# Kernel optimization log

Hardware: AMD Instinct MI355X
Metric: run time of the kernel (lower is better)

## Reference

```python
import jax, jax.numpy as jnp
import numpy as np

B, S, D, H, DFF = 4, 2048, 2048, 16, 8192
DH = D // H
THETA = 10000.0
EPS = 1e-5


def rmsnorm(x, g):
    return x * jax.lax.rsqrt(jnp.mean(x * x, axis=-1, keepdims=True) + EPS) * g


def rope(x, pos):
    # x: [B, H, S, DH]; rotate interleaved even/odd pairs
    half = DH // 2
    inv_freq = THETA ** (-(jnp.arange(half, dtype=jnp.float32) * 2.0) / DH)  # [half]
    ang = pos.astype(jnp.float32)[:, None] * inv_freq  # [S, half]
    cos, sin = jnp.cos(ang), jnp.sin(ang)
    x1, x2 = x[..., 0::2], x[..., 1::2]
    r1 = x1 * cos - x2 * sin
    r2 = x1 * sin + x2 * cos
    return jnp.stack([r1, r2], axis=-1).reshape(x.shape)


def setup_inputs() -> dict:
    key = jax.random.key(0)
    ks = jax.random.split(key, 12)
    s = 0.02
    return {
        "x": jax.random.normal(ks[0], (B, S, D), dtype=jnp.float32),
        "attention_mask": jnp.ones((S, S), dtype=bool),
        "wq": jax.random.normal(ks[1], (D, D), dtype=jnp.float32) * s,
        "wk": jax.random.normal(ks[2], (D, D), dtype=jnp.float32) * s,
        "wv": jax.random.normal(ks[3], (D, D), dtype=jnp.float32) * s,
        "wo": jax.random.normal(ks[4], (D, D), dtype=jnp.float32) * s,
        "w1": jax.random.normal(ks[5], (DFF, D), dtype=jnp.float32) * s,
        "w2": jax.random.normal(ks[6], (D, DFF), dtype=jnp.float32) * s,
        "w3": jax.random.normal(ks[7], (DFF, D), dtype=jnp.float32) * s,
        "g1": jnp.ones((D,), dtype=jnp.float32),
        "g2": jnp.ones((D,), dtype=jnp.float32),
    }


def reference(x, attention_mask, wq, wk, wv, wo, w1, w2, w3, g1, g2):
    pos = jnp.arange(x.shape[-2])
    # pre-norm attention
    h = rmsnorm(x, g1)
    q = (h @ wq.T).reshape(B, S, H, DH).transpose(0, 2, 1, 3)
    k = (h @ wk.T).reshape(B, S, H, DH).transpose(0, 2, 1, 3)
    v = (h @ wv.T).reshape(B, S, H, DH).transpose(0, 2, 1, 3)
    q = rope(q, pos)
    k = rope(k, pos)
    scores = jnp.einsum("bhqd,bhkd->bhqk", q, k) / np.float32(np.sqrt(DH))
    scores = jnp.where(attention_mask, scores, jnp.float32(-1e9))
    attn = jax.nn.softmax(scores, axis=-1)
    o = jnp.einsum("bhqk,bhkd->bhqd", attn, v)
    o = o.transpose(0, 2, 1, 3).reshape(B, S, D) @ wo.T
    x = x + o
    # pre-norm SwiGLU FFN
    h2 = rmsnorm(x, g2)
    ffn = (jax.nn.silu(h2 @ w1.T) * (h2 @ w3.T)) @ w2.T
    return x + ffn
```

## Files before the change

kernel.cpp:

```cpp
#include <hip/hip_runtime.h>
#include <cstdint>
#include <cstddef>

#define B_   4
#define S_   2048
#define D_   2048
#define H_   16
#define DH_  128
#define DFF_ 8192
#define LOG2E 1.4426950408889634f

typedef __bf16 bf16_t;
typedef __bf16 bf16x4 __attribute__((ext_vector_type(4)));
typedef __bf16 bf16x8 __attribute__((ext_vector_type(8)));
typedef float  f32x4  __attribute__((ext_vector_type(4)));

#define MFMA16 __builtin_amdgcn_mfma_f32_16x16x32_bf16

__device__ __forceinline__ void glds16(const void* g, void* l) {
  __builtin_amdgcn_global_load_lds((__attribute__((address_space(1))) void*)g,
                                   (__attribute__((address_space(3))) void*)l,
                                   16, 0, 0);
}

__global__ __launch_bounds__(256) void cvt_kernel(const float* __restrict__ in,
                                                  bf16_t* __restrict__ out, int n8) {
  int i = blockIdx.x * 256 + threadIdx.x;
  if (i >= n8) return;
  const float4* p4 = (const float4*)in;
  float4 a = p4[2 * (size_t)i];
  float4 b = p4[2 * (size_t)i + 1];
  bf16x8 o;
  o[0] = (bf16_t)a.x; o[1] = (bf16_t)a.y; o[2] = (bf16_t)a.z; o[3] = (bf16_t)a.w;
  o[4] = (bf16_t)b.x; o[5] = (bf16_t)b.y; o[6] = (bf16_t)b.z; o[7] = (bf16_t)b.w;
  ((bf16x8*)out)[i] = o;
}

__global__ __launch_bounds__(256) void rmsnorm_kernel(const float* __restrict__ x,
                                                      const float* __restrict__ g,
                                                      bf16_t* __restrict__ out) {
  const int row = blockIdx.x, tid = threadIdx.x;
  const float* xr = x + (size_t)row * D_;
  float4 a = ((const float4*)xr)[tid * 2];
  float4 b = ((const float4*)xr)[tid * 2 + 1];
  float ss = a.x*a.x + a.y*a.y + a.z*a.z + a.w*a.w
           + b.x*b.x + b.y*b.y + b.z*b.z + b.w*b.w;
#pragma unroll
  for (int m = 1; m < 64; m <<= 1) ss += __shfl_xor(ss, m);
  __shared__ float red[4];
  if ((tid & 63) == 0) red[tid >> 6] = ss;
  __syncthreads();
  float tot = red[0] + red[1] + red[2] + red[3];
  float rms = rsqrtf(tot * (1.0f / D_) + 1e-5f);
  float4 ga = ((const float4*)g)[tid * 2];
  float4 gb = ((const float4*)g)[tid * 2 + 1];
  bf16x8 o;
  o[0] = (bf16_t)(a.x * rms * ga.x); o[1] = (bf16_t)(a.y * rms * ga.y);
  o[2] = (bf16_t)(a.z * rms * ga.z); o[3] = (bf16_t)(a.w * rms * ga.w);
  o[4] = (bf16_t)(b.x * rms * gb.x); o[5] = (bf16_t)(b.y * rms * gb.y);
  o[6] = (bf16_t)(b.z * rms * gb.z); o[7] = (bf16_t)(b.w * rms * gb.w);
  ((bf16x8*)out)[(size_t)row * 256 + tid] = o;
}


#define RD_A(d, mg)                                                           \
  do {                                                                        \
    const char* p_ = ldsb + (d) * 32768 + wm * 16384 + l15 * 128 + (mg) * 8192; \
    _Pragma("unroll") for (int i_ = 0; i_ < 4; i_++) {                        \
      afr[i_][0] = *(const bf16x8*)(p_ + i_ * 2048 + acol0);                  \
      afr[i_][1] = *(const bf16x8*)(p_ + i_ * 2048 + acol1);                  \
    }                                                                         \
  } while (0)

#define RD_B(d, ng, dst)                                                      \
  do {                                                                        \
    const char* p_ = ldsb + 65536 + (d) * 32768 + (wn >> 1) * 16384 +         \
                     ((wn & 1) * 64 + l15) * 128 + (ng) * 4096;               \
    _Pragma("unroll") for (int j_ = 0; j_ < 2; j_++) {                        \
      dst[j_][0] = *(const bf16x8*)(p_ + j_ * 2048 + acol0);                  \
      dst[j_][1] = *(const bf16x8*)(p_ + j_ * 2048 + acol1);                  \
    }                                                                         \
  } while (0)

#define STAGE_A(d, kt)                                                        \
  do {                                                                        \
    char* dst_ = ldsb + (d) * 32768 + o0;                                     \
    const bf16_t* s_ = Asrc + (size_t)(kt) * 64;                              \
    glds16(s_, dst_);                                                         \
    glds16(s_ + 64 * (size_t)K, dst_ + 8192);                                 \
    glds16(s_ + 128 * (size_t)K, dst_ + 16384);                               \
    glds16(s_ + 192 * (size_t)K, dst_ + 24576);                               \
  } while (0)

#define STAGE_B(d, kt)                                                        \
  do {                                                                        \
    char* dst_ = ldsb + 65536 + (d) * 32768 + o0;                             \
    const bf16_t* s_ = Wsrc + (size_t)(kt) * 64;                              \
    glds16(s_, dst_);                                                         \
    glds16(s_ + 64 * (size_t)K, dst_ + 8192);                                 \
    glds16(s_ + 128 * (size_t)K, dst_ + 16384);                               \
    glds16(s_ + 192 * (size_t)K, dst_ + 24576);                               \
  } while (0)

#define DO_MFMA(mg, ng, bsrc)                                                 \
  do {                                                                        \
    __builtin_amdgcn_s_setprio(1);                                            \
    _Pragma("unroll") for (int i_ = 0; i_ < 4; i_++)                          \
    _Pragma("unroll") for (int j_ = 0; j_ < 2; j_++) {                        \
      acc[(mg)*4 + i_][(ng)*2 + j_] =                                         \
          MFMA16(afr[i_][0], bsrc[j_][0], acc[(mg)*4 + i_][(ng)*2 + j_], 0,0,0); \
      acc[(mg)*4 + i_][(ng)*2 + j_] =                                         \
          MFMA16(afr[i_][1], bsrc[j_][1], acc[(mg)*4 + i_][(ng)*2 + j_], 0,0,0); \
    }                                                                         \
    __builtin_amdgcn_s_setprio(0);                                            \
  } while (0)

#define PHASE_FENCE()                                                         \
  do {                                                                        \
    __builtin_amdgcn_sched_barrier(0);                                        \
    __builtin_amdgcn_s_barrier();                                             \
  } while (0)

template <int EPI>
__global__ __launch_bounds__(512, 2) void gemm256(const bf16_t* __restrict__ A,
                                                  const bf16_t* __restrict__ W,
                                                  const float* __restrict__ addf,
                                                  const bf16_t* __restrict__ addb,
                                                  bf16_t* __restrict__ outb,
                                                  bf16_t* __restrict__ outb2,
                                                  bf16_t* __restrict__ outb3,
                                                  float* __restrict__ outf,
                                                  int M, int N, int K) {
  __shared__ char ldsb[131072];
  const int tid = threadIdx.x;
  const int wid = tid >> 6, l = tid & 63, l15 = l & 15, lg = l >> 4;
  const int wm = wid >> 2, wn = wid & 3;

  const int nwg = gridDim.x;
  int wg = (int)blockIdx.x;
  wg = (wg & 7) * (nwg >> 3) + (wg >> 3);
  const int ntn = N >> 8;
  const int m0 = (wg / ntn) << 8, n0 = (wg % ntn) << 8;

  f32x4 acc[8][4];
  const f32x4 z4 = {0.f, 0.f, 0.f, 0.f};
#pragma unroll
  for (int i = 0; i < 8; i++)
#pragma unroll
    for (int j = 0; j < 4; j++) acc[i][j] = z4;

  const int o0 = tid * 16;
  const int srow = o0 >> 7;
  const int ssw = ((o0 & 127) ^ ((srow & 7) << 4)) >> 1;
  const bf16_t* Asrc = A + (size_t)(m0 + srow) * K + ssw;
  const bf16_t* Wsrc = W + (size_t)(n0 + srow) * K + ssw;

  const int rsw = (l15 & 7) << 4;
  const int acol0 = (lg * 16) ^ rsw;
  const int acol1 = (64 + lg * 16) ^ rsw;

  bf16x8 afr[4][2], bfr0[2][2], bfr1[2][2];

  const int NT = K >> 6;
  STAGE_A(0, 0);
  STAGE_B(0, 0);
  STAGE_A(1, 1);
  STAGE_B(1, 1);
  asm volatile("s_waitcnt vmcnt(8)" ::: "memory");
  __builtin_amdgcn_s_barrier();

  for (int t = 0; t < NT; t++) {
    const int d = t & 1;
    RD_A(d, 0);
    RD_B(d, 0, bfr0);
    PHASE_FENCE();
    DO_MFMA(0, 0, bfr0);
    PHASE_FENCE();
    RD_B(d, 1, bfr1);
    PHASE_FENCE();
    DO_MFMA(0, 1, bfr1);
    PHASE_FENCE();
    RD_A(d, 1);
    PHASE_FENCE();
    DO_MFMA(1, 1, bfr1);
    PHASE_FENCE();
    const bool pf2 = (t + 2 < NT);
    if (pf2) {
      STAGE_A(d, t + 2);
      STAGE_B(d, t + 2);
    }
    DO_MFMA(1, 0, bfr0);
    if (pf2) asm volatile("s_waitcnt vmcnt(8)" ::: "memory");
    else     asm volatile("s_waitcnt vmcnt(0)" ::: "memory");
    __builtin_amdgcn_sched_barrier(0);
    __builtin_amdgcn_s_barrier();
  }

#pragma unroll
  for (int m = 0; m < 8; m++) {
    const int gr = m0 + wm * 128 + m * 16 + lg * 4;
#pragma unroll
    for (int nn = 0; nn < 4; nn++) {
      const int gc = n0 + wn * 64 + nn * 16 + l15;
      if constexpr (EPI == 4) {
        const int seg = gc >> 11;
        const int gcl = gc & 2047;
        if (seg < 2) {
          bf16_t* o = seg ? outb2 : outb;
#pragma unroll
          for (int r = 0; r < 4; r++)
            o[(size_t)(gr + r) * D_ + gcl] = (bf16_t)acc[m][nn][r];
        } else {
          const int bb = gr >> 11, ss = gr & 2047;
          bf16x4 pk;
#pragma unroll
          for (int r = 0; r < 4; r++) pk[r] = (bf16_t)acc[m][nn][r];
          *(bf16x4*)(outb3 + ((size_t)bb * D_ + gcl) * S_ + ss) = pk;
        }
      } else {
#pragma unroll
        for (int r = 0; r < 4; r++) {
          size_t idx = (size_t)(gr + r) * N + gc;
          if constexpr (EPI == 0) {
            outb[idx] = (bf16_t)acc[m][nn][r];
          } else if constexpr (EPI == 1) {
            outf[idx] = acc[m][nn][r] + addf[idx];
          } else {
            float a1v = (float)addb[idx];
            outb[idx] = (bf16_t)(a1v / (1.0f + expf(-a1v)) * acc[m][nn][r]);
          }
        }
      }
    }
  }
}

__global__ __launch_bounds__(256) void rope_kernel(bf16_t* __restrict__ buf) {
  size_t i = (size_t)blockIdx.x * 256 + threadIdx.x;
  int pi = (int)(i & 63);
  size_t rh = i >> 6;
  int srow = (int)((rh / H_) % S_);
  float inv = expf((float)pi * (-9.210340371976184f / 64.0f));
  float ang = (float)srow * inv;
  float c = cosf(ang), sn = sinf(ang);
  bf16_t* p = buf + i * 2;
  float x1 = (float)p[0], x2 = (float)p[1];
  p[0] = (bf16_t)(x1 * c - x2 * sn);
  p[1] = (bf16_t)(x1 * sn + x2 * c);
}

__global__ __launch_bounds__(256) void attn_kernel(const bf16_t* __restrict__ Q,
                                                   const bf16_t* __restrict__ Kb,
                                                   const bf16_t* __restrict__ Vt,
                                                   bf16_t* __restrict__ O) {
  const int qt = blockIdx.x, h = blockIdx.y, b = blockIdx.z;
  const int tid = threadIdx.x;
  const int wid = tid >> 6, l = tid & 63, l15 = l & 15, lg = l >> 4;

  __shared__ bf16_t Klds[32 * 128];
  __shared__ bf16_t Vlds[128 * 32];
  __shared__ bf16_t Plds[4][16 * 40];

  const int q0 = qt * 64 + wid * 16;
  const f32x4 z4 = {0.f, 0.f, 0.f, 0.f};

  bf16x8 qf[4];
  {
    const bf16_t* qp = Q + ((size_t)(b * S_ + q0 + l15)) * D_ + h * DH_ + lg * 8;
#pragma unroll
    for (int kk = 0; kk < 4; kk++) qf[kk] = *(const bf16x8*)(qp + kk * 32);
  }
  f32x4 of[8];
#pragma unroll
  for (int f = 0; f < 8; f++) of[f] = z4;
  float m_run = -1e30f, l_run = 0.f;

  const int o0 = tid * 16;
  const int krow0 = o0 >> 8;
  const int kcolb = o0 & 255;
  const int scol = (kcolb ^ ((krow0 & 7) << 4)) >> 1;
  const int vrow0 = o0 >> 6;
  const int vc = (o0 >> 4) & 3;
  const int vcol = (vc ^ ((vrow0 >> 1) & 3)) << 3;
  const int vxor = (l15 >> 1) & 3;

  const size_t bh_off = ((size_t)b * S_) * D_ + (size_t)h * DH_;
  const bf16_t* vtbase = Vt + ((size_t)b * D_ + h * DH_) * S_;

  for (int kv0 = 0; kv0 < S_; kv0 += 32) {
    const bf16_t* kbase = Kb + bh_off + (size_t)kv0 * D_;
    glds16(kbase + (size_t)krow0 * D_ + scol,        (char*)Klds + wid * 1024);
    glds16(kbase + (size_t)(krow0 + 16) * D_ + scol, (char*)Klds + wid * 1024 + 4096);
    glds16(vtbase + (size_t)vrow0 * S_ + kv0 + vcol,        (char*)Vlds + wid * 1024);
    glds16(vtbase + (size_t)(vrow0 + 64) * S_ + kv0 + vcol, (char*)Vlds + wid * 1024 + 4096);
    __syncthreads();

    f32x4 st[2];
#pragma unroll
    for (int c = 0; c < 2; c++) {
      st[c] = z4;
      const int row = c * 16 + l15;
      const char* kr = (const char*)Klds + row * 256;
      const int sw = (row & 7) << 4;
#pragma unroll
      for (int kk = 0; kk < 4; kk++) {
        bf16x8 kf = *(const bf16x8*)(kr + ((kk * 64 + lg * 16) ^ sw));
        st[c] = MFMA16(kf, qf[kk], st[c], 0, 0, 0);
      }
    }

    float s[8];
#pragma unroll
    for (int c = 0; c < 2; c++)
#pragma unroll
      for (int r = 0; r < 4; r++) s[c * 4 + r] = st[c][r] * 0.08838834764831845f;
    float pm = s[0];
#pragma unroll
    for (int i = 1; i < 8; i++) pm = fmaxf(pm, s[i]);
    pm = fmaxf(pm, __shfl_xor(pm, 16));
    pm = fmaxf(pm, __shfl_xor(pm, 32));
    float mnew = fmaxf(m_run, pm);
    float alpha = exp2f((m_run - mnew) * LOG2E);
    float p[8], ts = 0.f;
#pragma unroll
    for (int i = 0; i < 8; i++) { p[i] = exp2f((s[i] - mnew) * LOG2E); ts += p[i]; }
    ts += __shfl_xor(ts, 16);
    ts += __shfl_xor(ts, 32);
    l_run = l_run * alpha + ts;
    m_run = mnew;

    float aq[4];
#pragma unroll
    for (int r = 0; r < 4; r++) aq[r] = __shfl(alpha, lg * 4 + r);
#pragma unroll
    for (int f = 0; f < 8; f++)
#pragma unroll
      for (int r = 0; r < 4; r++) of[f][r] *= aq[r];

    bf16_t* pw = &Plds[wid][0];
#pragma unroll
    for (int c = 0; c < 2; c++)
#pragma unroll
      for (int r = 0; r < 4; r++)
        pw[l15 * 40 + c * 16 + lg * 4 + r] = (bf16_t)p[c * 4 + r];
    asm volatile("s_waitcnt lgkmcnt(0)" ::: "memory");
    bf16x8 pa = *(const bf16x8*)(pw + l15 * 40 + lg * 8);
#pragma unroll
    for (int f = 0; f < 8; f++) {
      bf16x8 bv = *(const bf16x8*)((const char*)Vlds + (16 * f + l15) * 64 +
                                   ((lg ^ vxor) << 4));
      of[f] = MFMA16(pa, bv, of[f], 0, 0, 0);
    }
    __syncthreads();
  }

  float inv[4];
#pragma unroll
  for (int r = 0; r < 4; r++) inv[r] = 1.0f / __shfl(l_run, lg * 4 + r);
#pragma unroll
  for (int f = 0; f < 8; f++)
#pragma unroll
    for (int r = 0; r < 4; r++)
      O[((size_t)(b * S_ + q0 + lg * 4 + r)) * D_ + h * DH_ + 16 * f + l15] =
          (bf16_t)(of[f][r] * inv[r]);
}

extern "C" void kernel_launch(void* const* d_in, const int* in_sizes, int n_in,
                              void* d_out, int out_size, void* d_ws, size_t ws_size,
                              hipStream_t stream) {
  const float* x  = (const float*)d_in[0];
  const float* wq = (const float*)d_in[2];
  const float* wk = (const float*)d_in[3];
  const float* wv = (const float*)d_in[4];
  const float* wo = (const float*)d_in[5];
  const float* w1 = (const float*)d_in[6];
  const float* w2 = (const float*)d_in[7];
  const float* w3 = (const float*)d_in[8];
  const float* g1 = (const float*)d_in[9];
  const float* g2 = (const float*)d_in[10];
  float* out = (float*)d_out;

  const size_t ND = (size_t)D_ * D_;
  const size_t NF = (size_t)DFF_ * D_;
  const size_t SLOT = NF * 2;
  char* base = (char*)d_ws;
  bf16_t* wslot = (bf16_t*)(base);
  bf16_t* h1    = (bf16_t*)(base + 1 * SLOT);
  bf16_t* qb    = (bf16_t*)(base + 2 * SLOT);
  bf16_t* kb    = (bf16_t*)(base + 3 * SLOT);
  bf16_t* vt    = (bf16_t*)(base + 4 * SLOT);
  bf16_t* ob    = (bf16_t*)(base + 5 * SLOT);
  bf16_t* h2    = h1;
  bf16_t* g     = qb;
  float*  x1    = out;

  auto cvt = [&](const float* in, bf16_t* o, size_t n) {
    int n8 = (int)(n / 8);
    cvt_kernel<<<(n8 + 255) / 256, 256, 0, stream>>>(in, o, n8);
  };

  rmsnorm_kernel<<<B_ * S_, 256, 0, stream>>>(x, g1, h1);

  cvt(wq, wslot, ND);
  cvt(wk, wslot + ND, ND);
  cvt(wv, wslot + 2 * ND, ND);
  const int gqkv3 = (8192 / 256) * (6144 / 256);
  gemm256<4><<<gqkv3, 512, 0, stream>>>(h1, wslot, nullptr, nullptr,
                                        qb, kb, vt, nullptr, 8192, 6144, 2048);

  rope_kernel<<<(B_ * S_ * H_ * 64) / 256, 256, 0, stream>>>(qb);
  rope_kernel<<<(B_ * S_ * H_ * 64) / 256, 256, 0, stream>>>(kb);

  dim3 ga(S_ / 64, H_, B_);
  attn_kernel<<<ga, 256, 0, stream>>>(qb, kb, vt, ob);

  const int gqkv = (8192 / 256) * (2048 / 256);
  cvt(wo, wslot, ND);
  gemm256<1><<<gqkv, 512, 0, stream>>>(ob, wslot, x, nullptr,
                                       nullptr, nullptr, nullptr, x1, 8192, 2048, 2048);

  rmsnorm_kernel<<<B_ * S_, 256, 0, stream>>>(x1, g2, h2);

  const int gff = (8192 / 256) * (8192 / 256);
  cvt(w1, wslot, NF);
  gemm256<0><<<gff, 512, 0, stream>>>(h2, wslot, nullptr, nullptr,
                                      g, nullptr, nullptr, nullptr, 8192, 8192, 2048);

  cvt(w3, wslot, NF);
  gemm256<2><<<gff, 512, 0, stream>>>(h2, wslot, nullptr, g,
                                      g, nullptr, nullptr, nullptr, 8192, 8192, 2048);

  cvt(w2, wslot, NF);
  gemm256<1><<<gqkv, 512, 0, stream>>>(g, wslot, x1, nullptr,
                                       nullptr, nullptr, nullptr, x1, 8192, 2048, 8192);
}
```

Baseline: 1.497 ms.

## Use 1x8 wave layout and split stage loads across four MFMA phases

Changes the 256x256 GEMM wave tiling from a 2x4 grid (128x64 per wave) to a 1x8 grid, so each wave computes 256 rows by 32 columns. The K loop becomes four phases, each reading one 64-row slice of A. The global-to-LDS staging is split into half-tile loads spread over those phases, with the A upper half loaded only one tile ahead. The aim is to spread global load issue more evenly and overlap it with MFMA work. The cost is more LDS reads per wave, because every wave now reads the whole A tile, and a shorter prefetch distance for part of A.

```diff
diff --git a/kernel.cpp b/kernel.cpp
--- a/kernel.cpp
+++ b/kernel.cpp
@@ -63,54 +63,63 @@
 }
 
 
-#define RD_A(d, mg)                                                           \
-  do {                                                                        \
-    const char* p_ = ldsb + (d) * 32768 + wm * 16384 + l15 * 128 + (mg) * 8192; \
+#define RD_A_S(d, s)                                                          \
+  do {                                                                        \
+    const char* p_ = ldsb + (d) * 32768 + ((s) * 64 + l15) * 128;             \
     _Pragma("unroll") for (int i_ = 0; i_ < 4; i_++) {                        \
       afr[i_][0] = *(const bf16x8*)(p_ + i_ * 2048 + acol0);                  \
       afr[i_][1] = *(const bf16x8*)(p_ + i_ * 2048 + acol1);                  \
     }                                                                         \
   } while (0)
 
-#define RD_B(d, ng, dst)                                                      \
-  do {                                                                        \
-    const char* p_ = ldsb + 65536 + (d) * 32768 + (wn >> 1) * 16384 +         \
-                     ((wn & 1) * 64 + l15) * 128 + (ng) * 4096;               \
+#define RD_B(d)                                                               \
+  do {                                                                        \
+    const char* p_ = ldsb + 65536 + (d) * 32768 + (wn * 32 + l15) * 128;      \
     _Pragma("unroll") for (int j_ = 0; j_ < 2; j_++) {                        \
-      dst[j_][0] = *(const bf16x8*)(p_ + j_ * 2048 + acol0);                  \
-      dst[j_][1] = *(const bf16x8*)(p_ + j_ * 2048 + acol1);                  \
+      bfr[j_][0] = *(const bf16x8*)(p_ + j_ * 2048 + acol0);                  \
+      bfr[j_][1] = *(const bf16x8*)(p_ + j_ * 2048 + acol1);                  \
     }                                                                         \
   } while (0)
 
-#define STAGE_A(d, kt)                                                        \
+#define STAGE_A_LO(d, kt)                                                     \
   do {                                                                        \
     char* dst_ = ldsb + (d) * 32768 + o0;                                     \
     const bf16_t* s_ = Asrc + (size_t)(kt) * 64;                              \
     glds16(s_, dst_);                                                         \
     glds16(s_ + 64 * (size_t)K, dst_ + 8192);                                 \
-    glds16(s_ + 128 * (size_t)K, dst_ + 16384);                               \
-    glds16(s_ + 192 * (size_t)K, dst_ + 24576);                               \
-  } while (0)
-
-#define STAGE_B(d, kt)                                                        \
+  } while (0)
+
+#define STAGE_A_HI(d, kt)                                                     \
+  do {                                                                        \
+    char* dst_ = ldsb + (d) * 32768 + 16384 + o0;                             \
+    const bf16_t* s_ = Asrc + (size_t)(kt) * 64 + 128 * (size_t)K;            \
+    glds16(s_, dst_);                                                         \
+    glds16(s_ + 64 * (size_t)K, dst_ + 8192);                                 \
+  } while (0)
+
+#define STAGE_B_LO(d, kt)                                                     \
   do {                                                                        \
     char* dst_ = ldsb + 65536 + (d) * 32768 + o0;                             \
     const bf16_t* s_ = Wsrc + (size_t)(kt) * 64;                              \
     glds16(s_, dst_);                                                         \
     glds16(s_ + 64 * (size_t)K, dst_ + 8192);                                 \
-    glds16(s_ + 128 * (size_t)K, dst_ + 16384);                               \
-    glds16(s_ + 192 * (size_t)K, dst_ + 24576);                               \
-  } while (0)
-
-#define DO_MFMA(mg, ng, bsrc)                                                 \
+  } while (0)
+
+#define STAGE_B_HI(d, kt)                                                     \
+  do {                                                                        \
+    char* dst_ = ldsb + 65536 + (d) * 32768 + 16384 + o0;                     \
+    const bf16_t* s_ = Wsrc + (size_t)(kt) * 64 + 128 * (size_t)K;            \
+    glds16(s_, dst_);                                                         \
+    glds16(s_ + 64 * (size_t)K, dst_ + 8192);                                 \
+  } while (0)
+
+#define MFMA_S(s)                                                             \
   do {                                                                        \
     __builtin_amdgcn_s_setprio(1);                                            \
     _Pragma("unroll") for (int i_ = 0; i_ < 4; i_++)                          \
     _Pragma("unroll") for (int j_ = 0; j_ < 2; j_++) {                        \
-      acc[(mg)*4 + i_][(ng)*2 + j_] =                                         \
-          MFMA16(afr[i_][0], bsrc[j_][0], acc[(mg)*4 + i_][(ng)*2 + j_], 0,0,0); \
-      acc[(mg)*4 + i_][(ng)*2 + j_] =                                         \
-          MFMA16(afr[i_][1], bsrc[j_][1], acc[(mg)*4 + i_][(ng)*2 + j_], 0,0,0); \
+      acc[(s)*4 + i_][j_] = MFMA16(afr[i_][0], bfr[j_][0], acc[(s)*4 + i_][j_], 0,0,0); \
+      acc[(s)*4 + i_][j_] = MFMA16(afr[i_][1], bfr[j_][1], acc[(s)*4 + i_][j_], 0,0,0); \
     }                                                                         \
     __builtin_amdgcn_s_setprio(0);                                            \
   } while (0)
@@ -134,7 +143,7 @@
   __shared__ char ldsb[131072];
   const int tid = threadIdx.x;
   const int wid = tid >> 6, l = tid & 63, l15 = l & 15, lg = l >> 4;
-  const int wm = wid >> 2, wn = wid & 3;
+  const int wn = wid;
 
   const int nwg = gridDim.x;
   int wg = (int)blockIdx.x;
@@ -142,12 +151,10 @@
   const int ntn = N >> 8;
   const int m0 = (wg / ntn) << 8, n0 = (wg % ntn) << 8;
 
-  f32x4 acc[8][4];
+  f32x4 acc[16][2];
   const f32x4 z4 = {0.f, 0.f, 0.f, 0.f};
 #pragma unroll
-  for (int i = 0; i < 8; i++)
-#pragma unroll
-    for (int j = 0; j < 4; j++) acc[i][j] = z4;
+  for (int i = 0; i < 16; i++) { acc[i][0] = z4; acc[i][1] = z4; }
 
   const int o0 = tid * 16;
   const int srow = o0 >> 7;
@@ -159,49 +166,48 @@
   const int acol0 = (lg * 16) ^ rsw;
   const int acol1 = (64 + lg * 16) ^ rsw;
 
-  bf16x8 afr[4][2], bfr0[2][2], bfr1[2][2];
+  bf16x8 afr[4][2], bfr[2][2];
 
   const int NT = K >> 6;
-  STAGE_A(0, 0);
-  STAGE_B(0, 0);
-  STAGE_A(1, 1);
-  STAGE_B(1, 1);
-  asm volatile("s_waitcnt vmcnt(8)" ::: "memory");
+  STAGE_A_LO(0, 0); STAGE_A_HI(0, 0); STAGE_B_LO(0, 0); STAGE_B_HI(0, 0);
+  STAGE_B_LO(1, 1); STAGE_A_LO(1, 1); STAGE_B_HI(1, 1);
+  asm volatile("s_waitcnt vmcnt(6)" ::: "memory");
   __builtin_amdgcn_s_barrier();
 
   for (int t = 0; t < NT; t++) {
     const int d = t & 1;
-    RD_A(d, 0);
-    RD_B(d, 0, bfr0);
-    PHASE_FENCE();
-    DO_MFMA(0, 0, bfr0);
-    PHASE_FENCE();
-    RD_B(d, 1, bfr1);
-    PHASE_FENCE();
-    DO_MFMA(0, 1, bfr1);
-    PHASE_FENCE();
-    RD_A(d, 1);
-    PHASE_FENCE();
-    DO_MFMA(1, 1, bfr1);
-    PHASE_FENCE();
-    const bool pf2 = (t + 2 < NT);
-    if (pf2) {
-      STAGE_A(d, t + 2);
-      STAGE_B(d, t + 2);
-    }
-    DO_MFMA(1, 0, bfr0);
-    if (pf2) asm volatile("s_waitcnt vmcnt(8)" ::: "memory");
-    else     asm volatile("s_waitcnt vmcnt(0)" ::: "memory");
+    RD_B(d);
+    RD_A_S(d, 0);
+    if (t + 1 < NT) STAGE_A_HI(d ^ 1, t + 1);
+    PHASE_FENCE();
+    MFMA_S(0);
+    PHASE_FENCE();
+    RD_A_S(d, 1);
+    if (t + 2 < NT) STAGE_B_LO(d, t + 2);
+    PHASE_FENCE();
+    MFMA_S(1);
+    PHASE_FENCE();
+    RD_A_S(d, 2);
+    if (t + 2 < NT) STAGE_A_LO(d, t + 2);
+    PHASE_FENCE();
+    MFMA_S(2);
+    PHASE_FENCE();
+    RD_A_S(d, 3);
+    if (t + 2 < NT) STAGE_B_HI(d, t + 2);
+    PHASE_FENCE();
+    MFMA_S(3);
+    if (t + 2 < NT) asm volatile("s_waitcnt vmcnt(6)" ::: "memory");
+    else            asm volatile("s_waitcnt vmcnt(0)" ::: "memory");
     __builtin_amdgcn_sched_barrier(0);
     __builtin_amdgcn_s_barrier();
   }
 
 #pragma unroll
-  for (int m = 0; m < 8; m++) {
-    const int gr = m0 + wm * 128 + m * 16 + lg * 4;
-#pragma unroll
-    for (int nn = 0; nn < 4; nn++) {
-      const int gc = n0 + wn * 64 + nn * 16 + l15;
+  for (int m = 0; m < 16; m++) {
+    const int gr = m0 + m * 16 + lg * 4;
+#pragma unroll
+    for (int nn = 0; nn < 2; nn++) {
+      const int gc = n0 + wn * 32 + nn * 16 + l15;
       if constexpr (EPI == 4) {
         const int seg = gc >> 11;
         const int gcl = gc & 2047;
```

Result: slower. 1.528 ms (+2.1%).
